# Optimization experiments

Hardware: AMD Instinct MI355X
Metric: run time of the kernel (lower is better)

Reference implementation:

```python
import jax, jax.numpy as jnp
import numpy as np

CUTOFF = 5.0
NUM_RADIAL = 6
HIDDEN = 128
N_NODES = 100000
N_EDGES = 800000
MAX_Z = 95
P = 6  # envelope_exponent(5) + 1, per PyG Envelope


def _envelope(x):
    # PyG DimeNet Envelope: (1/x + a*x^(p-1) + b*x^p + c*x^(p+1)) * (x < 1)
    a = -(P + 1) * (P + 2) / 2.0   # -28
    b = P * (P + 2)                # 48
    c = -P * (P + 1) / 2.0         # -21
    xp0 = x ** (P - 1)
    xp1 = xp0 * x
    xp2 = xp1 * x
    return (1.0 / x + a * xp0 + b * xp1 + c * xp2) * (x < 1.0)


def setup_inputs():
    key = jax.random.key(0)
    ks = jax.random.split(key, 8)
    z = jax.random.randint(ks[0], (N_NODES,), 0, MAX_Z, dtype=jnp.int32)
    pos = jax.random.normal(ks[1], (N_NODES, 3), dtype=jnp.float32)
    ei = jax.random.randint(ks[2], (2, N_EDGES), 0, N_NODES, dtype=jnp.int32)
    i, j = ei[0], ei[1]
    j = jnp.where(j == i, (j + 1) % N_NODES, j)  # radius_graph emits no self-loops (avoids d=0)
    edge_index = jnp.stack([i, j])
    # BesselBasisLayer learnable frequencies: pi * n
    freq = np.pi * jnp.arange(1, NUM_RADIAL + 1, dtype=jnp.float32)
    s3 = float(np.sqrt(3.0))
    emb_table = jax.random.uniform(ks[3], (MAX_Z, HIDDEN), jnp.float32, -s3, s3)
    W_rbf = jax.random.normal(ks[4], (NUM_RADIAL, HIDDEN), jnp.float32) * (1.0 / np.sqrt(NUM_RADIAL))
    b_rbf = jnp.zeros((HIDDEN,), jnp.float32)
    W_lin = jax.random.normal(ks[5], (3 * HIDDEN, HIDDEN), jnp.float32) * (1.0 / np.sqrt(3 * HIDDEN))
    b_lin = jnp.zeros((HIDDEN,), jnp.float32)
    return {"z": z, "pos": pos, "edge_index": edge_index, "freq": freq,
            "emb_table": emb_table, "W_rbf": W_rbf, "b_rbf": b_rbf,
            "W_lin": W_lin, "b_lin": b_lin}


def reference(z, pos, edge_index, freq, emb_table, W_rbf, b_rbf, W_lin, b_lin):
    n = z.shape[0]
    i, j = edge_index[0], edge_index[1]
    # per-edge distance  [E]
    d = jnp.sqrt(jnp.sum((pos[i] - pos[j]) ** 2, axis=-1))
    # Bessel RBF  [E, num_radial]
    x = d[:, None] / CUTOFF
    rbf = _envelope(x) * jnp.sin(freq * x)
    # DimeNet EmbeddingBlock (act = SiLU/swish)
    h_rbf = jax.nn.silu(rbf @ W_rbf + b_rbf)            # [E, H]
    xz = emb_table[z]                                    # [N, H]
    e_emb = jax.nn.silu(
        jnp.concatenate([xz[i], xz[j], h_rbf], axis=-1) @ W_lin + b_lin
    )                                                    # [E, H]
    # scatter_mean over target node j -> [N, H]
    sums = jax.ops.segment_sum(e_emb, j, num_segments=n)
    cnt = jax.ops.segment_sum(jnp.ones_like(d), j, num_segments=n)
    v_emb = sums / jnp.maximum(cnt, 1.0)[:, None]
    return v_emb  # pool=None -> node-level embeddings
```

## Files before the change

### kernel.cpp

```cpp
#include <hip/hip_runtime.h>
#include <hip/hip_bf16.h>
#include <math.h>

#define HID 128
#define NRAD 6
#define TABN 4096
#define CUTOFF_INV 0.2f
#define MZ 95
#define PAD 32
#define OVF_CAP 65536
#define FTR 8

typedef unsigned int uint32;

__global__ void build1(const float* __restrict__ emb, const float* __restrict__ W_lin,
                       const float* __restrict__ freq, const float* __restrict__ W_rbf,
                       const float* __restrict__ b_rbf, const float* __restrict__ b_lin,
                       const int* __restrict__ ei, const float* __restrict__ pos,
                       const int* __restrict__ z,
                       __hip_bfloat16* __restrict__ Tb, float* __restrict__ ftab,
                       int* __restrict__ cnt, int* __restrict__ payload,
                       int* __restrict__ ovfcnt, int2* __restrict__ ovfbuf,
                       int MAXZ, int E) {
    __shared__ float sh[FTR * HID];
    int h   = threadIdx.x;
    int bid = blockIdx.x;
    int nT  = 2 * MAXZ;
    int nF  = (TABN + FTR) / FTR;
    if (bid < nT) {
        int zz = bid >> 1, s = bid & 1;
        sh[h] = emb[zz * HID + h];
        __syncthreads();
        const float* W = W_lin + (size_t)s * HID * HID;
        float acc = (s == 0) ? b_lin[h] : 0.f;
#pragma unroll 8
        for (int k = 0; k < HID; ++k) acc = fmaf(sh[k], W[k * HID + h], acc);
        Tb[(size_t)(s * MAXZ + zz) * HID + h] = __float2bfloat16(acc);
    } else if (bid < nT + nF) {
        int t0 = (bid - nT) * FTR;
        for (int r = 0; r < FTR; ++r) {
            int t = t0 + r;
            float rbf[NRAD];
            if (t == 0) {
#pragma unroll
                for (int k = 0; k < NRAD; ++k) rbf[k] = freq[k];
            } else if (t >= TABN) {
#pragma unroll
                for (int k = 0; k < NRAD; ++k) rbf[k] = 0.f;
            } else {
                float x  = (float)t / (float)TABN;
                float x2 = x * x, x5 = x2 * x2 * x;
                float env = 1.f / x + x5 * (-28.f + x * (48.f + x * (-21.f)));
#pragma unroll
                for (int k = 0; k < NRAD; ++k) rbf[k] = env * sinf(freq[k] * x);
            }
            float pre = b_rbf[h];
#pragma unroll
            for (int k = 0; k < NRAD; ++k) pre = fmaf(rbf[k], W_rbf[k * HID + h], pre);
            sh[r * HID + h] = pre / (1.f + __expf(-pre));
        }
        __syncthreads();
        const float* W3 = W_lin + (size_t)2 * HID * HID;
        float acc[FTR];
#pragma unroll
        for (int r = 0; r < FTR; ++r) acc[r] = 0.f;
#pragma unroll 4
        for (int k = 0; k < HID; ++k) {
            float w = W3[k * HID + h];
#pragma unroll
            for (int r = 0; r < FTR; ++r) acc[r] = fmaf(sh[r * HID + k], w, acc[r]);
        }
        for (int r = 0; r < FTR; ++r) {
            int t = t0 + r;
            if (t <= TABN) ftab[(size_t)t * HID + h] = acc[r];
        }
    } else {
        int e = (bid - nT - nF) * HID + h;
        if (e < E) {
            int i = ei[e];
            int j = ei[E + e];
            float dx = pos[3 * i]     - pos[3 * j];
            float dy = pos[3 * i + 1] - pos[3 * j + 1];
            float dz = pos[3 * i + 2] - pos[3 * j + 2];
            float d  = sqrtf(dx * dx + dy * dy + dz * dz);
            float u  = fminf(d * CUTOFF_INV, 1.0f) * (float)TABN;
            int   ti = (int)(u + 0.5f);
            if (ti > TABN) ti = TABN;
            int pl = ti | (z[i] << 13) | (z[j] << 20);
            int r  = atomicAdd(&cnt[j], 1);
            if (r < PAD) {
                payload[(size_t)j * PAD + r] = pl;
            } else {
                int o = atomicAdd(ovfcnt, 1);
                if (o < OVF_CAP) ovfbuf[o] = make_int2(j, pl);
            }
        }
    }
}

#define EDGE_ACC(pl_) do {                                                                    \
    int ti_ = (pl_) & 0x1FFF;                                                                 \
    int zi_ = ((pl_) >> 13) & 0x7F;                                                           \
    int zj_ = ((pl_) >> 20) & 0x7F;                                                           \
    float4 f_ = *(const float4*)(ftab + (size_t)ti_ * HID + h4);                              \
    uint32 a0_ = sT[zi_ * (HID / 2) + l2];                                                    \
    uint32 a1_ = sT[zi_ * (HID / 2) + l2 + 1];                                                \
    uint32 b0_ = sT[(MZ + zj_) * (HID / 2) + l2];                                             \
    uint32 b1_ = sT[(MZ + zj_) * (HID / 2) + l2 + 1];                                         \
    float p0_ = __uint_as_float(a0_ << 16)         + __uint_as_float(b0_ << 16)         + f_.x; \
    float p1_ = __uint_as_float(a0_ & 0xFFFF0000u) + __uint_as_float(b0_ & 0xFFFF0000u) + f_.y; \
    float p2_ = __uint_as_float(a1_ << 16)         + __uint_as_float(b1_ << 16)         + f_.z; \
    float p3_ = __uint_as_float(a1_ & 0xFFFF0000u) + __uint_as_float(b1_ & 0xFFFF0000u) + f_.w; \
    ax = fmaf(p0_, __builtin_amdgcn_rcpf(1.f + __expf(-p0_)), ax);                            \
    ay = fmaf(p1_, __builtin_amdgcn_rcpf(1.f + __expf(-p1_)), ay);                            \
    az = fmaf(p2_, __builtin_amdgcn_rcpf(1.f + __expf(-p2_)), az);                            \
    aw = fmaf(p3_, __builtin_amdgcn_rcpf(1.f + __expf(-p3_)), aw);                            \
} while (0)

__launch_bounds__(1024)
__global__ void gather_k(const int* __restrict__ cnt, const int* __restrict__ payload,
                         const uint32* __restrict__ Tb32, const float* __restrict__ ftab,
                         const int* __restrict__ ovfcnt, const int2* __restrict__ ovfbuf,
                         float* __restrict__ out, int N) {
    __shared__ uint32 sT[2 * MZ * (HID / 2)];
    int tid = threadIdx.x;
    for (int k = tid; k < 2 * MZ * (HID / 2); k += 1024) sT[k] = Tb32[k];
    __syncthreads();

    int lane = tid & 63, wv = tid >> 6;
    int hi   = (lane >> 5) & 1;
    int l32  = lane & 31;
    int h4   = l32 * 4;
    int l2   = l32 * 2;
    int nCh  = (N + 31) >> 5;
    int nov  = *ovfcnt;
    if (nov > OVF_CAP) nov = OVF_CAP;

    for (int ch = blockIdx.x; ch < nCh; ch += gridDim.x) {
        int nA = (ch << 5) + (wv << 1);
        if (nA >= N) continue;
        int  n      = nA + hi;
        bool nvalid = (n < N);
        int deg = 0, plv = 0;
        if (nvalid) {
            deg = cnt[n];
            plv = payload[(size_t)n * PAD + l32];
        }
        int cb  = deg < PAD ? deg : PAD;
        int cbA = __builtin_amdgcn_readlane(cb, 0);
        int cbB = __builtin_amdgcn_readlane(cb, 32);
        int cbm = cbA > cbB ? cbA : cbB;

        float ax = 0.f, ay = 0.f, az = 0.f, aw = 0.f;
        for (int k = 0; k < cbm; ++k) {
            int plA = __builtin_amdgcn_readlane(plv, k);
            int plB = __builtin_amdgcn_readlane(plv, k + 32);
            int pl  = hi ? plB : plA;
            if (k < cb) {
                EDGE_ACC(pl);
            }
        }
        if (deg > PAD && nov > 0) {
            for (int o = 0; o < nov; ++o) {
                int2 v = ovfbuf[o];
                if (v.x == n) { int pl = v.y; EDGE_ACC(pl); }
            }
        }
        if (nvalid) {
            float s = (deg > 0) ? 1.0f / (float)deg : 0.0f;
            float4 o4;
            o4.x = ax * s; o4.y = ay * s; o4.z = az * s; o4.w = aw * s;
            *(float4*)(out + (size_t)n * HID + h4) = o4;
        }
    }
}

extern "C" void kernel_launch(void* const* d_in, const int* in_sizes, int n_in,
                              void* d_out, int out_size, void* d_ws, size_t ws_size,
                              hipStream_t stream) {
    const int*   z     = (const int*)d_in[0];
    const float* pos   = (const float*)d_in[1];
    const int*   ei    = (const int*)d_in[2];
    const float* freq  = (const float*)d_in[3];
    const float* emb   = (const float*)d_in[4];
    const float* W_rbf = (const float*)d_in[5];
    const float* b_rbf = (const float*)d_in[6];
    const float* W_lin = (const float*)d_in[7];
    const float* b_lin = (const float*)d_in[8];

    int N    = in_sizes[0];
    int E    = in_sizes[2] / 2;
    int MAXZ = in_sizes[4] / HID;
    float* out = (float*)d_out;

    int N_pad = ((N + 1024) / 1024) * 1024;

    char* ws = (char*)d_ws;
    size_t off = 0;
    auto alloc = [&](size_t bytes) { char* p = ws + off; off = (off + bytes + 255) & ~(size_t)255; return p; };
    int*   cnt     = (int*)alloc((size_t)N_pad * 4);
    int*   ovfcnt  = (int*)alloc(256);
    __hip_bfloat16* Tb = (__hip_bfloat16*)alloc((size_t)2 * MAXZ * HID * 2);
    float* ftab    = (float*)alloc((size_t)(TABN + 1) * HID * 4);
    int*   payload = (int*)alloc((size_t)N_pad * PAD * 4);
    int2*  ovfbuf  = (int2*)alloc((size_t)OVF_CAP * 8);

    hipMemsetAsync(cnt, 0, (size_t)N_pad * 4 + 256, stream);

    int nBuild = 2 * MAXZ + (TABN + FTR) / FTR + (E + HID - 1) / HID;
    build1<<<nBuild, HID, 0, stream>>>(emb, W_lin, freq, W_rbf, b_rbf, b_lin,
                                       ei, pos, z, Tb, ftab, cnt, payload,
                                       ovfcnt, ovfbuf, MAXZ, E);
    gather_k<<<512, 1024, 0, stream>>>(cnt, payload, (const uint32*)Tb, ftab,
                                       ovfcnt, ovfbuf, out, N);
}
```

Before: 190.3 us.

## Split each node's edges across wave halves with sentinel padding and xor-shuffle reduction

The gather kernel now gives one node to each wave. The two 32-lane halves process alternating edges and combine their results with a cross-half shuffle, where before each half handled its own node. Padding lanes get a sentinel payload that points to an extra Tb row filled with -60, so SiLU yields about zero, which removes the per-edge predicate. This is meant to reduce the loop imbalance between the two nodes sharing a wave and to shorten the per-node iteration count. The cost is twice as many wave iterations per node plus a shuffle reduction, and the sentinel contributes only approximately zero, not exactly zero.

```diff
diff --git a/kernel.cpp b/kernel.cpp
--- a/kernel.cpp
+++ b/kernel.cpp
@@ -7,6 +7,8 @@
 #define TABN 4096
 #define CUTOFF_INV 0.2f
 #define MZ 95
+#define MZP (MZ + 1)
+#define SENT ((MZ << 13) | (MZ << 20))
 #define PAD 32
 #define OVF_CAP 65536
 #define FTR 8
@@ -25,17 +27,21 @@
     __shared__ float sh[FTR * HID];
     int h   = threadIdx.x;
     int bid = blockIdx.x;
-    int nT  = 2 * MAXZ;
+    int nT  = 2 * (MAXZ + 1);
     int nF  = (TABN + FTR) / FTR;
     if (bid < nT) {
         int zz = bid >> 1, s = bid & 1;
+        if (zz == MAXZ) {
+            Tb[(size_t)(s * (MAXZ + 1) + zz) * HID + h] = __float2bfloat16(-60.0f);
+            return;
+        }
         sh[h] = emb[zz * HID + h];
         __syncthreads();
         const float* W = W_lin + (size_t)s * HID * HID;
         float acc = (s == 0) ? b_lin[h] : 0.f;
 #pragma unroll 8
         for (int k = 0; k < HID; ++k) acc = fmaf(sh[k], W[k * HID + h], acc);
-        Tb[(size_t)(s * MAXZ + zz) * HID + h] = __float2bfloat16(acc);
+        Tb[(size_t)(s * (MAXZ + 1) + zz) * HID + h] = __float2bfloat16(acc);
     } else if (bid < nT + nF) {
         int t0 = (bid - nT) * FTR;
         for (int r = 0; r < FTR; ++r) {
@@ -102,11 +108,11 @@
     int ti_ = (pl_) & 0x1FFF;                                                                 \
     int zi_ = ((pl_) >> 13) & 0x7F;                                                           \
     int zj_ = ((pl_) >> 20) & 0x7F;                                                           \
-    float4 f_ = *(const float4*)(ftab + (size_t)ti_ * HID + h4);                              \
+    float4 f_ = *(const float4*)((const char*)ftab + (uint32)((ti_ << 9) + fb4));             \
     uint32 a0_ = sT[zi_ * (HID / 2) + l2];                                                    \
     uint32 a1_ = sT[zi_ * (HID / 2) + l2 + 1];                                                \
-    uint32 b0_ = sT[(MZ + zj_) * (HID / 2) + l2];                                             \
-    uint32 b1_ = sT[(MZ + zj_) * (HID / 2) + l2 + 1];                                         \
+    uint32 b0_ = sT[(MZP + zj_) * (HID / 2) + l2];                                            \
+    uint32 b1_ = sT[(MZP + zj_) * (HID / 2) + l2 + 1];                                        \
     float p0_ = __uint_as_float(a0_ << 16)         + __uint_as_float(b0_ << 16)         + f_.x; \
     float p1_ = __uint_as_float(a0_ & 0xFFFF0000u) + __uint_as_float(b0_ & 0xFFFF0000u) + f_.y; \
     float p2_ = __uint_as_float(a1_ << 16)         + __uint_as_float(b1_ << 16)         + f_.z; \
@@ -122,43 +128,34 @@
                          const uint32* __restrict__ Tb32, const float* __restrict__ ftab,
                          const int* __restrict__ ovfcnt, const int2* __restrict__ ovfbuf,
                          float* __restrict__ out, int N) {
-    __shared__ uint32 sT[2 * MZ * (HID / 2)];
+    __shared__ uint32 sT[2 * MZP * (HID / 2)];
     int tid = threadIdx.x;
-    for (int k = tid; k < 2 * MZ * (HID / 2); k += 1024) sT[k] = Tb32[k];
+    for (int k = tid; k < 2 * MZP * (HID / 2); k += 1024) sT[k] = Tb32[k];
     __syncthreads();
 
     int lane = tid & 63, wv = tid >> 6;
-    int hi   = (lane >> 5) & 1;
+    int hi   = lane >> 5;
     int l32  = lane & 31;
     int h4   = l32 * 4;
     int l2   = l32 * 2;
-    int nCh  = (N + 31) >> 5;
+    uint32 fb4 = (uint32)h4 << 2;
     int nov  = *ovfcnt;
     if (nov > OVF_CAP) nov = OVF_CAP;
-
-    for (int ch = blockIdx.x; ch < nCh; ch += gridDim.x) {
-        int nA = (ch << 5) + (wv << 1);
-        if (nA >= N) continue;
-        int  n      = nA + hi;
-        bool nvalid = (n < N);
-        int deg = 0, plv = 0;
-        if (nvalid) {
-            deg = cnt[n];
-            plv = payload[(size_t)n * PAD + l32];
-        }
+    int nW = gridDim.x << 4;
+
+    for (int n = (blockIdx.x << 4) + wv; n < N; n += nW) {
+        int deg = cnt[n];
+        int plv = payload[(size_t)n * PAD + l32];
         int cb  = deg < PAD ? deg : PAD;
-        int cbA = __builtin_amdgcn_readlane(cb, 0);
-        int cbB = __builtin_amdgcn_readlane(cb, 32);
-        int cbm = cbA > cbB ? cbA : cbB;
+        plv = (l32 < cb) ? plv : SENT;
+        int nit = (cb + 1) >> 1;
 
         float ax = 0.f, ay = 0.f, az = 0.f, aw = 0.f;
-        for (int k = 0; k < cbm; ++k) {
-            int plA = __builtin_amdgcn_readlane(plv, k);
-            int plB = __builtin_amdgcn_readlane(plv, k + 32);
+        for (int k = 0; k < nit; ++k) {
+            int plA = __builtin_amdgcn_readlane(plv, 2 * k);
+            int plB = __builtin_amdgcn_readlane(plv, 2 * k + 1);
             int pl  = hi ? plB : plA;
-            if (k < cb) {
-                EDGE_ACC(pl);
-            }
+            EDGE_ACC(pl);
         }
         if (deg > PAD && nov > 0) {
             for (int o = 0; o < nov; ++o) {
@@ -166,7 +163,11 @@
                 if (v.x == n) { int pl = v.y; EDGE_ACC(pl); }
             }
         }
-        if (nvalid) {
+        ax += __shfl_xor(ax, 32);
+        ay += __shfl_xor(ay, 32);
+        az += __shfl_xor(az, 32);
+        aw += __shfl_xor(aw, 32);
+        if (hi == 0) {
             float s = (deg > 0) ? 1.0f / (float)deg : 0.0f;
             float4 o4;
             o4.x = ax * s; o4.y = ay * s; o4.z = az * s; o4.w = aw * s;
@@ -200,14 +201,14 @@
     auto alloc = [&](size_t bytes) { char* p = ws + off; off = (off + bytes + 255) & ~(size_t)255; return p; };
     int*   cnt     = (int*)alloc((size_t)N_pad * 4);
     int*   ovfcnt  = (int*)alloc(256);
-    __hip_bfloat16* Tb = (__hip_bfloat16*)alloc((size_t)2 * MAXZ * HID * 2);
+    __hip_bfloat16* Tb = (__hip_bfloat16*)alloc((size_t)2 * (MAXZ + 1) * HID * 2);
     float* ftab    = (float*)alloc((size_t)(TABN + 1) * HID * 4);
     int*   payload = (int*)alloc((size_t)N_pad * PAD * 4);
     int2*  ovfbuf  = (int2*)alloc((size_t)OVF_CAP * 8);
 
     hipMemsetAsync(cnt, 0, (size_t)N_pad * 4 + 256, stream);
 
-    int nBuild = 2 * MAXZ + (TABN + FTR) / FTR + (E + HID - 1) / HID;
+    int nBuild = 2 * (MAXZ + 1) + (TABN + FTR) / FTR + (E + HID - 1) / HID;
     build1<<<nBuild, HID, 0, stream>>>(emb, W_lin, freq, W_rbf, b_rbf, b_lin,
                                        ei, pos, z, Tb, ftab, cnt, payload,
                                        ovfcnt, ovfbuf, MAXZ, E);
```

After: 186.8 us. About the same (-1.8%).
